# Optimization experiments

Hardware: AMD Instinct MI355X
Metric: run time of the kernel (lower is better)

The kernel has to match this reference:

```python
import jax, jax.numpy as jnp
import numpy as np

BATCH, IN, OUT = 8192, 4096, 4096


def setup_inputs() -> dict:
    key = jax.random.key(0)
    k1, k2, k3 = jax.random.split(key, 3)
    x = jax.random.normal(k1, (BATCH, IN), dtype=jnp.float32)
    weight = jax.random.normal(k2, (OUT, IN), dtype=jnp.float32)
    bias = jax.random.normal(k3, (OUT,), dtype=jnp.float32)
    return {"x": x, "weight": weight, "bias": bias}


def reference(x, weight, bias):
    # Binarize weights/bias with sign (matches torch.sign: sign(0)=0), then fp32 GEMM + bias add.
    w = jnp.sign(weight)            # [OUT, IN], values in {-1, 0, +1}
    b = jnp.sign(bias)              # [OUT]
    return jnp.dot(x, w.T) + b[None, :]   # [BATCH, OUT]
```

## Files before the change

kernel.cpp:

```cpp
#include <hip/hip_runtime.h>
#include <stdint.h>
#include <stddef.h>


#define MDIM 8192
#define NDIM 4096
#define KDIM 4096
#define NT   (KDIM / 64)

typedef __attribute__((ext_vector_type(8))) short bf16x8;
typedef __attribute__((ext_vector_type(4))) float f32x4;

__device__ __forceinline__ short f2bf(float f) {
  union { float f; unsigned u; } a; a.f = f;
  unsigned r = a.u + 0x7FFFu + ((a.u >> 16) & 1u);
  return (short)(r >> 16);
}

__device__ __forceinline__ float fsign(float x) {
  return (x > 0.f) ? 1.f : ((x < 0.f) ? -1.f : 0.f);
}

__device__ __forceinline__ short signbf(float x) {
  return (x > 0.f) ? (short)0x3F80 : ((x < 0.f) ? (short)0xBF80 : (short)0);
}

__device__ __forceinline__ void gl_lds16(const void* g, void* l) {
  __builtin_amdgcn_global_load_lds(
      (const __attribute__((address_space(1))) unsigned*)g,
      (__attribute__((address_space(3))) unsigned*)l,
      16, 0, 0);
}


__global__ void cvt_x_kernel(const float* __restrict__ x, short* __restrict__ o) {
  int i = blockIdx.x * blockDim.x + threadIdx.x;
  float4 v = ((const float4*)x)[i];
  short4 s;
  s.x = f2bf(v.x); s.y = f2bf(v.y); s.z = f2bf(v.z); s.w = f2bf(v.w);
  ((short4*)o)[i] = s;
}

__global__ void cvt_w_kernel(const float* __restrict__ w, short* __restrict__ o) {
  int i = blockIdx.x * blockDim.x + threadIdx.x;
  float4 v = ((const float4*)w)[i];
  short4 s;
  s.x = signbf(v.x); s.y = signbf(v.y); s.z = signbf(v.z); s.w = signbf(v.w);
  ((short4*)o)[i] = s;
}


#define STAGE(BUF, HH, KTS) do {                                               \
    const short* _s = ((HH) < 2 ? aA + (size_t)((HH) * 128) * KDIM             \
                                : aB + (size_t)(((HH) - 2) * 128) * KDIM)      \
                      + (size_t)(KTS) * 64;                                    \
    char* _d = ldst + (BUF) * 65536 + (HH) * 16384;                            \
    gl_lds16(_s, _d);                                                          \
    gl_lds16(_s + (size_t)64 * KDIM, _d + 8192);                               \
  } while (0)

#define READ_A(QOFF) do {                                                      \
    _Pragma("unroll") for (int i = 0; i < 4; ++i) {                            \
      const int ro = so + arow + (QOFF) + i * 2048;                            \
      a[i][0] = *(const bf16x8*)(sm + ro + colp0);                             \
      a[i][1] = *(const bf16x8*)(sm + ro + colp1);                             \
    } } while (0)

#define READ_B(DST, QOFF) do {                                                 \
    _Pragma("unroll") for (int j = 0; j < 2; ++j) {                            \
      const int ro = so + brow + (QOFF) + j * 2048;                            \
      DST[j][0] = *(const bf16x8*)(sm + ro + colp0);                           \
      DST[j][1] = *(const bf16x8*)(sm + ro + colp1);                           \
    } } while (0)

#define MFMA_Q(I0, J0, BREG) do {                                              \
    __builtin_amdgcn_s_setprio(1);                                            \
    _Pragma("unroll") for (int i = 0; i < 4; ++i)                              \
      _Pragma("unroll") for (int j = 0; j < 2; ++j) {                          \
        acc[(I0) + i][(J0) + j] = __builtin_amdgcn_mfma_f32_16x16x32_bf16(     \
            a[i][0], BREG[j][0], acc[(I0) + i][(J0) + j], 0, 0, 0);            \
        acc[(I0) + i][(J0) + j] = __builtin_amdgcn_mfma_f32_16x16x32_bf16(     \
            a[i][1], BREG[j][1], acc[(I0) + i][(J0) + j], 0, 0, 0);            \
      }                                                                        \
    __builtin_amdgcn_s_setprio(0);                                            \
  } while (0)

#define SYNC_PRE_MFMA() do {                                                   \
    __builtin_amdgcn_s_barrier();                                              \
    asm volatile("s_waitcnt lgkmcnt(0)" ::: "memory");                         \
    __builtin_amdgcn_sched_barrier(0);                                         \
  } while (0)

__global__ __launch_bounds__(512, 2) void gemm_8phase(
    const short* __restrict__ A,
    const short* __restrict__ B,
    const float* __restrict__ bias,
    float* __restrict__ C) {
  __shared__ __align__(16) char sm[131072];

  const int t    = threadIdx.x;
  const int lane = t & 63;
  const int w    = t >> 6;
  const int wm   = w >> 2;
  const int wn   = w & 3;
  const int fr   = lane & 15;
  const int g    = lane >> 4;

  const int bid = blockIdx.y * gridDim.x + blockIdx.x;
  const int swz = (bid & 7) * 64 + (bid >> 3);
  const int bm  = (swz >> 4) << 8;
  const int bn  = (swz & 15) << 8;

  const int sx    = (fr & 7) << 4;
  const int colp0 = (g << 4) ^ sx;
  const int colp1 = (64 | (g << 4)) ^ sx;
  const int arow  = (wm * 128 + fr) * 128;
  const int brow  = 32768 + (wn * 64 + fr) * 128;

  const int srow = t >> 3;
  const int scol = ((t & 7) ^ (srow & 7)) << 3;
  const short* aA = A + (size_t)(bm + srow) * KDIM + scol;
  const short* aB = B + (size_t)(bn + srow) * KDIM + scol;
  char* ldst = (char*)sm + t * 16;

  f32x4 acc[8][4] = {};
  bf16x8 a[4][2], b0[2][2], b1[2][2];

  STAGE(0, 0, 0);
  STAGE(0, 1, 0);
  STAGE(0, 2, 0);
  STAGE(0, 3, 0);
  STAGE(1, 0, 1);
  asm volatile("s_waitcnt vmcnt(2)" ::: "memory");
  __builtin_amdgcn_s_barrier();

  for (int kt = 0; kt < NT; ++kt) {
    const int so = (kt & 1) << 16;
    const int nb = (kt & 1) ^ 1;
    const int cb = (kt & 1);

    READ_A(0);
    READ_B(b0, 0);
    if (kt + 1 < NT) STAGE(nb, 1, kt + 1);
    SYNC_PRE_MFMA();
    MFMA_Q(0, 0, b0);
    __builtin_amdgcn_s_barrier();

    READ_B(b1, 4096);
    if (kt + 1 < NT) STAGE(nb, 2, kt + 1);
    SYNC_PRE_MFMA();
    MFMA_Q(0, 2, b1);
    __builtin_amdgcn_s_barrier();

    READ_A(8192);
    if (kt + 1 < NT) STAGE(nb, 3, kt + 1);
    SYNC_PRE_MFMA();
    MFMA_Q(4, 2, b1);
    __builtin_amdgcn_s_barrier();

    if (kt + 2 < NT) STAGE(cb, 0, kt + 2);
    __builtin_amdgcn_s_barrier();
    MFMA_Q(4, 0, b0);
    if (kt + 2 < NT) {
      asm volatile("s_waitcnt vmcnt(2)" ::: "memory");
    } else {
      asm volatile("s_waitcnt vmcnt(0)" ::: "memory");
    }
    __builtin_amdgcn_s_barrier();
  }

  const int crow = bm + wm * 128;
  const int ccol = bn + wn * 64 + fr;
#pragma unroll
  for (int jj = 0; jj < 4; ++jj) {
    const int gc = ccol + jj * 16;
    const float bs = fsign(bias[gc]);
#pragma unroll
    for (int ii = 0; ii < 8; ++ii) {
      float* cp = C + (size_t)(crow + ii * 16 + g * 4) * NDIM + gc;
#pragma unroll
      for (int r = 0; r < 4; ++r)
        cp[(size_t)r * NDIM] = acc[ii][jj][r] + bs;
    }
  }
}


__global__ __launch_bounds__(256) void gemm_fused(
    const float* __restrict__ A,
    const float* __restrict__ W,
    const float* __restrict__ bias,
    float* __restrict__ C) {
  __shared__ short As[128 * 32];
  __shared__ short Bs[128 * 32];

  const int t    = threadIdx.x;
  const int lane = t & 63;
  const int wm   = (t >> 6) >> 1;
  const int wn   = (t >> 6) & 1;

  const int bm = blockIdx.y * 128;
  const int bn = blockIdx.x * 128;

  f32x4 acc[4][4] = {};

  const int srow = t >> 1;
  const int scol = (t & 1) << 4;

  const float* pA = A + (size_t)(bm + srow) * KDIM + scol;
  const float* pW = W + (size_t)(bn + srow) * KDIM + scol;
  short* sA = As + srow * 32 + scol;
  short* sB = Bs + srow * 32 + scol;

  const int fr  = lane & 15;
  const int fkB = (lane >> 4) << 4;

  for (int k0 = 0; k0 < KDIM; k0 += 32) {
    float4 va[4], vb[4];
#pragma unroll
    for (int q = 0; q < 4; ++q) {
      va[q] = *(const float4*)(pA + k0 + q * 4);
      vb[q] = *(const float4*)(pW + k0 + q * 4);
    }
    __syncthreads();
    short va_s[16], vb_s[16];
#pragma unroll
    for (int q = 0; q < 4; ++q) {
      va_s[q * 4 + 0] = f2bf(va[q].x); va_s[q * 4 + 1] = f2bf(va[q].y);
      va_s[q * 4 + 2] = f2bf(va[q].z); va_s[q * 4 + 3] = f2bf(va[q].w);
      vb_s[q * 4 + 0] = signbf(vb[q].x); vb_s[q * 4 + 1] = signbf(vb[q].y);
      vb_s[q * 4 + 2] = signbf(vb[q].z); vb_s[q * 4 + 3] = signbf(vb[q].w);
    }
    bf16x8 ca, cbv;
#pragma unroll
    for (int e = 0; e < 8; ++e) { ca[e] = va_s[e]; cbv[e] = vb_s[e]; }
    *(bf16x8*)(sA) = ca;
    *(bf16x8*)(sB) = cbv;
#pragma unroll
    for (int e = 0; e < 8; ++e) { ca[e] = va_s[8 + e]; cbv[e] = vb_s[8 + e]; }
    *(bf16x8*)(sA + 8) = ca;
    *(bf16x8*)(sB + 8) = cbv;
    __syncthreads();

    bf16x8 af[4], bfr[4];
#pragma unroll
    for (int i = 0; i < 4; ++i) {
      af[i]  = *(const bf16x8*)((const char*)As + (wm * 64 + i * 16 + fr) * 64 + fkB);
      bfr[i] = *(const bf16x8*)((const char*)Bs + (wn * 64 + i * 16 + fr) * 64 + fkB);
    }
#pragma unroll
    for (int i = 0; i < 4; ++i)
#pragma unroll
      for (int j = 0; j < 4; ++j)
        acc[i][j] = __builtin_amdgcn_mfma_f32_16x16x32_bf16(af[i], bfr[j], acc[i][j], 0, 0, 0);
  }
  __syncthreads();

  const int row0 = bm + wm * 64 + ((lane >> 4) << 2);
  const int col0 = bn + wn * 64 + (lane & 15);
#pragma unroll
  for (int j = 0; j < 4; ++j) {
    const int gc = col0 + j * 16;
    const float bs = fsign(bias[gc]);
#pragma unroll
    for (int i = 0; i < 4; ++i) {
      float* cp = C + (size_t)(row0 + i * 16) * NDIM + gc;
#pragma unroll
      for (int r = 0; r < 4; ++r)
        cp[(size_t)r * NDIM] = acc[i][j][r] + bs;
    }
  }
}

extern "C" void kernel_launch(void* const* d_in, const int* in_sizes, int n_in,
                              void* d_out, int out_size, void* d_ws, size_t ws_size,
                              hipStream_t stream) {
  const float* x    = (const float*)d_in[0];
  const float* w    = (const float*)d_in[1];
  const float* bias = (const float*)d_in[2];
  float* out = (float*)d_out;

  const size_t xb_bytes = (size_t)MDIM * KDIM * 2;
  const size_t wb_bytes = (size_t)NDIM * KDIM * 2;

  if (ws_size >= xb_bytes + wb_bytes) {
    short* xb = (short*)d_ws;
    short* wb = (short*)((char*)d_ws + xb_bytes);
    cvt_x_kernel<<<(MDIM * (KDIM / 4)) / 256, 256, 0, stream>>>(x, xb);
    cvt_w_kernel<<<(NDIM * (KDIM / 4)) / 256, 256, 0, stream>>>(w, wb);
    dim3 grid(NDIM / 256, MDIM / 256);
    gemm_8phase<<<grid, 512, 0, stream>>>(xb, wb, bias, out);
  } else {
    dim3 grid(NDIM / 128, MDIM / 128);
    gemm_fused<<<grid, 256, 0, stream>>>(x, w, bias, out);
  }
}
```

Baseline: 478.6 us.

## Merge conversion kernels and deepen GEMM prefetch to two stages ahead

The two fp32-to-bf16 conversion kernels become one grid-stride kernel with a fixed grid, saving a launch. The GEMM main loop now issues loads for two A/B halves at once, at the first and last phases, instead of spreading them over four phases. That keeps more loads in flight, with vmcnt waits raised from 2 to 4. This gives more prefetch depth ahead of the MFMAs, at the cost of burstier memory issue and possible LDS overlap hazards if the buffer regions being staged are still being read.

After: 497.3 us. 1.04x slower.

```diff
diff --git a/kernel.cpp b/kernel.cpp
--- a/kernel.cpp
+++ b/kernel.cpp
@@ -33,20 +33,26 @@
 }
 
 
-__global__ void cvt_x_kernel(const float* __restrict__ x, short* __restrict__ o) {
-  int i = blockIdx.x * blockDim.x + threadIdx.x;
-  float4 v = ((const float4*)x)[i];
-  short4 s;
-  s.x = f2bf(v.x); s.y = f2bf(v.y); s.z = f2bf(v.z); s.w = f2bf(v.w);
-  ((short4*)o)[i] = s;
-}
-
-__global__ void cvt_w_kernel(const float* __restrict__ w, short* __restrict__ o) {
-  int i = blockIdx.x * blockDim.x + threadIdx.x;
-  float4 v = ((const float4*)w)[i];
-  short4 s;
-  s.x = signbf(v.x); s.y = signbf(v.y); s.z = signbf(v.z); s.w = signbf(v.w);
-  ((short4*)o)[i] = s;
+#define XF4 (MDIM * (KDIM / 4))
+#define WF4 (NDIM * (KDIM / 4))
+
+__global__ void cvt_both(const float* __restrict__ x, const float* __restrict__ w,
+                         short* __restrict__ xb, short* __restrict__ wb) {
+  const int stride = gridDim.x * blockDim.x;
+  for (int i = blockIdx.x * blockDim.x + threadIdx.x; i < XF4 + WF4; i += stride) {
+    if (i < XF4) {
+      float4 v = ((const float4*)x)[i];
+      short4 s;
+      s.x = f2bf(v.x); s.y = f2bf(v.y); s.z = f2bf(v.z); s.w = f2bf(v.w);
+      ((short4*)xb)[i] = s;
+    } else {
+      int j = i - XF4;
+      float4 v = ((const float4*)w)[j];
+      short4 s;
+      s.x = signbf(v.x); s.y = signbf(v.y); s.z = signbf(v.z); s.w = signbf(v.w);
+      ((short4*)wb)[j] = s;
+    }
+  }
 }
 
 
@@ -131,7 +137,8 @@
   STAGE(0, 2, 0);
   STAGE(0, 3, 0);
   STAGE(1, 0, 1);
-  asm volatile("s_waitcnt vmcnt(2)" ::: "memory");
+  STAGE(1, 1, 1);
+  asm volatile("s_waitcnt vmcnt(4)" ::: "memory");
   __builtin_amdgcn_s_barrier();
 
   for (int kt = 0; kt < NT; ++kt) {
@@ -141,28 +148,32 @@
 
     READ_A(0);
     READ_B(b0, 0);
-    if (kt + 1 < NT) STAGE(nb, 1, kt + 1);
+    if (kt + 1 < NT) {
+      STAGE(nb, 2, kt + 1);
+      STAGE(nb, 3, kt + 1);
+    }
     SYNC_PRE_MFMA();
     MFMA_Q(0, 0, b0);
     __builtin_amdgcn_s_barrier();
 
     READ_B(b1, 4096);
-    if (kt + 1 < NT) STAGE(nb, 2, kt + 1);
     SYNC_PRE_MFMA();
     MFMA_Q(0, 2, b1);
     __builtin_amdgcn_s_barrier();
 
     READ_A(8192);
-    if (kt + 1 < NT) STAGE(nb, 3, kt + 1);
     SYNC_PRE_MFMA();
     MFMA_Q(4, 2, b1);
     __builtin_amdgcn_s_barrier();
 
-    if (kt + 2 < NT) STAGE(cb, 0, kt + 2);
+    if (kt + 2 < NT) {
+      STAGE(cb, 0, kt + 2);
+      STAGE(cb, 1, kt + 2);
+    }
     __builtin_amdgcn_s_barrier();
     MFMA_Q(4, 0, b0);
     if (kt + 2 < NT) {
-      asm volatile("s_waitcnt vmcnt(2)" ::: "memory");
+      asm volatile("s_waitcnt vmcnt(4)" ::: "memory");
     } else {
       asm volatile("s_waitcnt vmcnt(0)" ::: "memory");
     }
@@ -286,8 +297,7 @@
   if (ws_size >= xb_bytes + wb_bytes) {
     short* xb = (short*)d_ws;
     short* wb = (short*)((char*)d_ws + xb_bytes);
-    cvt_x_kernel<<<(MDIM * (KDIM / 4)) / 256, 256, 0, stream>>>(x, xb);
-    cvt_w_kernel<<<(NDIM * (KDIM / 4)) / 256, 256, 0, stream>>>(w, wb);
+    cvt_both<<<4096, 256, 0, stream>>>(x, w, xb, wb);
     dim3 grid(NDIM / 256, MDIM / 256);
     gemm_8phase<<<grid, 512, 0, stream>>>(xb, wb, bias, out);
   } else {
```

## Switch main GEMM to 32x32x16 bf16 MFMA with reworked staging schedule

Applied to the files above, without the earlier changes.

Replaces the 16x16x32 MFMA tiling with 32x32x16 bf16 MFMA instructions, so each wave holds 4x2 32x32 accumulator tiles and reads larger LDS fragments per instruction. The larger MFMA shape cuts LDS reads per FLOP and the number of issued instructions. The global-to-LDS staging is regrouped into pairs of half-tiles issued in two phases, with vmcnt thresholds adjusted to match. This changes the register footprint and the epilogue's output layout, which may affect occupancy and store coalescing.

New measurement: 513.6 us. 7.3% more time.

```diff
diff --git a/kernel.cpp b/kernel.cpp
--- a/kernel.cpp
+++ b/kernel.cpp
@@ -10,6 +10,7 @@
 
 typedef __attribute__((ext_vector_type(8))) short bf16x8;
 typedef __attribute__((ext_vector_type(4))) float f32x4;
+typedef __attribute__((ext_vector_type(16))) float f32x16;
 
 __device__ __forceinline__ short f2bf(float f) {
   union { float f; unsigned u; } a; a.f = f;
@@ -59,29 +60,25 @@
     gl_lds16(_s + (size_t)64 * KDIM, _d + 8192);                               \
   } while (0)
 
-#define READ_A(QOFF) do {                                                      \
-    _Pragma("unroll") for (int i = 0; i < 4; ++i) {                            \
-      const int ro = so + arow + (QOFF) + i * 2048;                            \
-      a[i][0] = *(const bf16x8*)(sm + ro + colp0);                             \
-      a[i][1] = *(const bf16x8*)(sm + ro + colp1);                             \
+#define READ_A32(DST, I0) do {                                                 \
+    _Pragma("unroll") for (int s = 0; s < 4; ++s) {                            \
+      const int cp = ((s << 5) | hb) ^ sx;                                     \
+      DST[0][s] = *(const bf16x8*)(sm + so + arowB + (I0) * 4096 + cp);        \
+      DST[1][s] = *(const bf16x8*)(sm + so + arowB + (I0) * 4096 + 4096 + cp); \
     } } while (0)
 
-#define READ_B(DST, QOFF) do {                                                 \
-    _Pragma("unroll") for (int j = 0; j < 2; ++j) {                            \
-      const int ro = so + brow + (QOFF) + j * 2048;                            \
-      DST[j][0] = *(const bf16x8*)(sm + ro + colp0);                           \
-      DST[j][1] = *(const bf16x8*)(sm + ro + colp1);                           \
+#define READ_B32(DST, J) do {                                                  \
+    _Pragma("unroll") for (int s = 0; s < 4; ++s) {                            \
+      const int cp = ((s << 5) | hb) ^ sx;                                     \
+      DST[s] = *(const bf16x8*)(sm + so + browB + (J) * 4096 + cp);            \
     } } while (0)
 
-#define MFMA_Q(I0, J0, BREG) do {                                              \
+#define MFMA32(I0, J, BV, AV) do {                                             \
     __builtin_amdgcn_s_setprio(1);                                            \
-    _Pragma("unroll") for (int i = 0; i < 4; ++i)                              \
-      _Pragma("unroll") for (int j = 0; j < 2; ++j) {                          \
-        acc[(I0) + i][(J0) + j] = __builtin_amdgcn_mfma_f32_16x16x32_bf16(     \
-            a[i][0], BREG[j][0], acc[(I0) + i][(J0) + j], 0, 0, 0);            \
-        acc[(I0) + i][(J0) + j] = __builtin_amdgcn_mfma_f32_16x16x32_bf16(     \
-            a[i][1], BREG[j][1], acc[(I0) + i][(J0) + j], 0, 0, 0);            \
-      }                                                                        \
+    _Pragma("unroll") for (int s = 0; s < 4; ++s)                              \
+      _Pragma("unroll") for (int ii = 0; ii < 2; ++ii)                         \
+        acc[(I0) + ii][J] = __builtin_amdgcn_mfma_f32_32x32x16_bf16(           \
+            AV[ii][s], BV[s], acc[(I0) + ii][J], 0, 0, 0);                     \
     __builtin_amdgcn_s_setprio(0);                                            \
   } while (0)
 
@@ -103,19 +100,18 @@
   const int w    = t >> 6;
   const int wm   = w >> 2;
   const int wn   = w & 3;
-  const int fr   = lane & 15;
-  const int g    = lane >> 4;
+  const int l31  = lane & 31;
+  const int hh   = lane >> 5;
+  const int hb   = hh << 4;
+  const int sx   = (lane & 7) << 4;
 
   const int bid = blockIdx.y * gridDim.x + blockIdx.x;
   const int swz = (bid & 7) * 64 + (bid >> 3);
   const int bm  = (swz >> 4) << 8;
   const int bn  = (swz & 15) << 8;
 
-  const int sx    = (fr & 7) << 4;
-  const int colp0 = (g << 4) ^ sx;
-  const int colp1 = (64 | (g << 4)) ^ sx;
-  const int arow  = (wm * 128 + fr) * 128;
-  const int brow  = 32768 + (wn * 64 + fr) * 128;
+  const int arowB = (wm * 128 + l31) * 128;
+  const int browB = 32768 + (wn * 64 + l31) * 128;
 
   const int srow = t >> 3;
   const int scol = ((t & 7) ^ (srow & 7)) << 3;
@@ -123,15 +119,16 @@
   const short* aB = B + (size_t)(bn + srow) * KDIM + scol;
   char* ldst = (char*)sm + t * 16;
 
-  f32x4 acc[8][4] = {};
-  bf16x8 a[4][2], b0[2][2], b1[2][2];
+  f32x16 acc[4][2] = {};
+  bf16x8 aLo[2][4], aHi[2][4], b0v[4], b1v[4];
 
   STAGE(0, 0, 0);
   STAGE(0, 1, 0);
   STAGE(0, 2, 0);
   STAGE(0, 3, 0);
   STAGE(1, 0, 1);
-  asm volatile("s_waitcnt vmcnt(2)" ::: "memory");
+  STAGE(1, 1, 1);
+  asm volatile("s_waitcnt vmcnt(4)" ::: "memory");
   __builtin_amdgcn_s_barrier();
 
   for (int kt = 0; kt < NT; ++kt) {
@@ -139,48 +136,54 @@
     const int nb = (kt & 1) ^ 1;
     const int cb = (kt & 1);
 
-    READ_A(0);
-    READ_B(b0, 0);
-    if (kt + 1 < NT) STAGE(nb, 1, kt + 1);
+    READ_A32(aLo, 0);
+    READ_B32(b0v, 0);
+    if (kt + 1 < NT) {
+      STAGE(nb, 2, kt + 1);
+      STAGE(nb, 3, kt + 1);
+    }
     SYNC_PRE_MFMA();
-    MFMA_Q(0, 0, b0);
-    __builtin_amdgcn_s_barrier();
-
-    READ_B(b1, 4096);
-    if (kt + 1 < NT) STAGE(nb, 2, kt + 1);
+    MFMA32(0, 0, b0v, aLo);
+    __builtin_amdgcn_s_barrier();
+
+    READ_B32(b1v, 1);
     SYNC_PRE_MFMA();
-    MFMA_Q(0, 2, b1);
-    __builtin_amdgcn_s_barrier();
-
-    READ_A(8192);
-    if (kt + 1 < NT) STAGE(nb, 3, kt + 1);
+    MFMA32(0, 1, b1v, aLo);
+    __builtin_amdgcn_s_barrier();
+
+    READ_A32(aHi, 2);
     SYNC_PRE_MFMA();
-    MFMA_Q(4, 2, b1);
-    __builtin_amdgcn_s_barrier();
-
-    if (kt + 2 < NT) STAGE(cb, 0, kt + 2);
-    __builtin_amdgcn_s_barrier();
-    MFMA_Q(4, 0, b0);
+    MFMA32(2, 1, b1v, aHi);
+    __builtin_amdgcn_s_barrier();
+
     if (kt + 2 < NT) {
-      asm volatile("s_waitcnt vmcnt(2)" ::: "memory");
+      STAGE(cb, 0, kt + 2);
+      STAGE(cb, 1, kt + 2);
+    }
+    __builtin_amdgcn_s_barrier();
+    MFMA32(2, 0, b0v, aHi);
+    if (kt + 2 < NT) {
+      asm volatile("s_waitcnt vmcnt(4)" ::: "memory");
     } else {
       asm volatile("s_waitcnt vmcnt(0)" ::: "memory");
     }
     __builtin_amdgcn_s_barrier();
   }
 
-  const int crow = bm + wm * 128;
-  const int ccol = bn + wn * 64 + fr;
-#pragma unroll
-  for (int jj = 0; jj < 4; ++jj) {
-    const int gc = ccol + jj * 16;
+  const int crow = bm + wm * 128 + hh * 4;
+  const int ccol = bn + wn * 64 + l31;
+#pragma unroll
+  for (int j = 0; j < 2; ++j) {
+    const int gc = ccol + j * 32;
     const float bs = fsign(bias[gc]);
 #pragma unroll
-    for (int ii = 0; ii < 8; ++ii) {
-      float* cp = C + (size_t)(crow + ii * 16 + g * 4) * NDIM + gc;
-#pragma unroll
-      for (int r = 0; r < 4; ++r)
-        cp[(size_t)r * NDIM] = acc[ii][jj][r] + bs;
+    for (int ii = 0; ii < 4; ++ii) {
+      const int rbase = crow + ii * 32;
+#pragma unroll
+      for (int reg = 0; reg < 16; ++reg) {
+        const int row = rbase + (reg & 3) + 8 * (reg >> 2);
+        C[(size_t)row * NDIM + gc] = acc[ii][j][reg] + bs;
+      }
     }
   }
 }
```

## Unroll K loop by two and rebalance global-to-LDS prefetch schedule

Applied to the files above, without the earlier changes.

Unrolls the K-tile loop by two so the LDS buffer offsets become compile-time constants. It also regroups the global-to-LDS staging. Two quarters of the next tile are now issued together in the first phase, and two quarters of the tile after next are issued in the last phase. Before, one quarter was issued per phase. The vmcnt waits are adjusted to match, which gives half of each A tile a full extra iteration of prefetch slack. The cost is more outstanding loads bunched together and larger code.

Result: slower. 509.4 us (+6.4%).

```diff
diff --git a/kernel.cpp b/kernel.cpp
--- a/kernel.cpp
+++ b/kernel.cpp
@@ -59,16 +59,16 @@
     gl_lds16(_s + (size_t)64 * KDIM, _d + 8192);                               \
   } while (0)
 
-#define READ_A(QOFF) do {                                                      \
+#define READ_A(SO, QOFF) do {                                                  \
     _Pragma("unroll") for (int i = 0; i < 4; ++i) {                            \
-      const int ro = so + arow + (QOFF) + i * 2048;                            \
+      const int ro = (SO) + arow + (QOFF) + i * 2048;                          \
       a[i][0] = *(const bf16x8*)(sm + ro + colp0);                             \
       a[i][1] = *(const bf16x8*)(sm + ro + colp1);                             \
     } } while (0)
 
-#define READ_B(DST, QOFF) do {                                                 \
+#define READ_B(SO, DST, QOFF) do {                                             \
     _Pragma("unroll") for (int j = 0; j < 2; ++j) {                            \
-      const int ro = so + brow + (QOFF) + j * 2048;                            \
+      const int ro = (SO) + brow + (QOFF) + j * 2048;                          \
       DST[j][0] = *(const bf16x8*)(sm + ro + colp0);                           \
       DST[j][1] = *(const bf16x8*)(sm + ro + colp1);                           \
     } } while (0)
@@ -91,6 +91,42 @@
     __builtin_amdgcn_sched_barrier(0);                                         \
   } while (0)
 
+#define KTILE(SO, CBUF, NBUF, KT) do {                                         \
+                                                        \
+    READ_A(SO, 0);                                                             \
+    READ_B(SO, b0, 0);                                                         \
+    if ((KT) + 1 < NT) {                                                       \
+      STAGE(NBUF, 2, (KT) + 1);                                                \
+      STAGE(NBUF, 3, (KT) + 1);                                                \
+    }                                                                          \
+    SYNC_PRE_MFMA();                                                           \
+    MFMA_Q(0, 0, b0);                                                          \
+    __builtin_amdgcn_s_barrier();                                              \
+                                                        \
+    READ_B(SO, b1, 4096);                                                      \
+    SYNC_PRE_MFMA();                                                           \
+    MFMA_Q(0, 2, b1);                                                          \
+    __builtin_amdgcn_s_barrier();                                              \
+                                                        \
+    READ_A(SO, 8192);                                                          \
+    SYNC_PRE_MFMA();                                                           \
+    MFMA_Q(4, 2, b1);                                                          \
+    __builtin_amdgcn_s_barrier();                                              \
+                                                        \
+    if ((KT) + 2 < NT) {                                                       \
+      STAGE(CBUF, 0, (KT) + 2);                                                \
+      STAGE(CBUF, 1, (KT) + 2);                                                \
+    }                                                                          \
+    __builtin_amdgcn_s_barrier();                                              \
+    MFMA_Q(4, 0, b0);                                                          \
+    if ((KT) + 2 < NT) {                                                       \
+      asm volatile("s_waitcnt vmcnt(4)" ::: "memory");                         \
+    } else {                                                                   \
+      asm volatile("s_waitcnt vmcnt(0)" ::: "memory");                         \
+    }                                                                          \
+    __builtin_amdgcn_s_barrier();                                              \
+  } while (0)
+
 __global__ __launch_bounds__(512, 2) void gemm_8phase(
     const short* __restrict__ A,
     const short* __restrict__ B,
@@ -131,42 +167,13 @@
   STAGE(0, 2, 0);
   STAGE(0, 3, 0);
   STAGE(1, 0, 1);
-  asm volatile("s_waitcnt vmcnt(2)" ::: "memory");
+  STAGE(1, 1, 1);
+  asm volatile("s_waitcnt vmcnt(4)" ::: "memory");
   __builtin_amdgcn_s_barrier();
 
-  for (int kt = 0; kt < NT; ++kt) {
-    const int so = (kt & 1) << 16;
-    const int nb = (kt & 1) ^ 1;
-    const int cb = (kt & 1);
-
-    READ_A(0);
-    READ_B(b0, 0);
-    if (kt + 1 < NT) STAGE(nb, 1, kt + 1);
-    SYNC_PRE_MFMA();
-    MFMA_Q(0, 0, b0);
-    __builtin_amdgcn_s_barrier();
-
-    READ_B(b1, 4096);
-    if (kt + 1 < NT) STAGE(nb, 2, kt + 1);
-    SYNC_PRE_MFMA();
-    MFMA_Q(0, 2, b1);
-    __builtin_amdgcn_s_barrier();
-
-    READ_A(8192);
-    if (kt + 1 < NT) STAGE(nb, 3, kt + 1);
-    SYNC_PRE_MFMA();
-    MFMA_Q(4, 2, b1);
-    __builtin_amdgcn_s_barrier();
-
-    if (kt + 2 < NT) STAGE(cb, 0, kt + 2);
-    __builtin_amdgcn_s_barrier();
-    MFMA_Q(4, 0, b0);
-    if (kt + 2 < NT) {
-      asm volatile("s_waitcnt vmcnt(2)" ::: "memory");
-    } else {
-      asm volatile("s_waitcnt vmcnt(0)" ::: "memory");
-    }
-    __builtin_amdgcn_s_barrier();
+  for (int kt = 0; kt < NT; kt += 2) {
+    KTILE(0,     0, 1, kt);
+    KTILE(65536, 1, 0, kt + 1);
   }
 
   const int crow = bm + wm * 128;
```
